# Performance work log

Measured on AMD Instinct MI355X. Metric: run time of the kernel, lower is better.

The kernel has to match this reference:

```python
import jax, jax.numpy as jnp
import numpy as np

P = 16          # patch size
D = 256         # emb dim
NH = 4          # attention heads
DH = D // NH    # head dim
GS = 4          # LE-fusion group size
EPS = 1e-5
ALPHA = 1.0
DELTA = 1.0
BETA = 1.0


def setup_inputs() -> dict:
    key = jax.random.key(0)
    ks = jax.random.split(key, 12)
    B, C, H, W = 8, 1, 256, 256
    s = 0.02
    return {
        "x": jax.random.normal(ks[0], (B, C, H, W), jnp.float32),
        # patch embed as matmul over flattened patches (equivalent to Conv2d k=s=P)
        "Wp": jax.random.normal(ks[1], (C * P * P, D), jnp.float32) * s,
        "bp": jnp.zeros((D,), jnp.float32),
        "ln_g": jnp.ones((D,), jnp.float32),
        "ln_b": jnp.zeros((D,), jnp.float32),
        "Wq": jax.random.normal(ks[2], (D, D), jnp.float32) * s,
        "bq": jnp.zeros((D,), jnp.float32),
        "Wk": jax.random.normal(ks[3], (D, D), jnp.float32) * s,
        "bk": jnp.zeros((D,), jnp.float32),
        "Wv": jax.random.normal(ks[4], (D, D), jnp.float32) * s,
        "bv": jnp.zeros((D,), jnp.float32),
        "Wo": jax.random.normal(ks[5], (D, D), jnp.float32) * s,
        "bo": jnp.zeros((D,), jnp.float32),
    }


def _forward(x, Wp, bp, ln_g, ln_b, Wq, bq, Wk, bk, Wv, bv, Wo, bo):
    B, C, H, W = x.shape
    nh, nw = H // P, W // P
    N = nh * nw
    # --- patch embed: (B,C,H,W) -> (B,N,C*P*P) @ Wp ---
    patches = x.reshape(B, C, nh, P, nw, P).transpose(0, 2, 4, 1, 3, 5)
    patches = patches.reshape(B, N, C * P * P)
    z = patches @ Wp + bp  # (B, N, D)
    # --- NF-Norm: LayerNorm then NeuroFocal scaling ---
    mu = z.mean(-1, keepdims=True)
    var = ((z - mu) ** 2).mean(-1, keepdims=True)
    zn = (z - mu) * jax.lax.rsqrt(var + EPS) * ln_g + ln_b
    mu2 = zn.mean(-1, keepdims=True)
    var2 = ((zn - mu2) ** 2).mean(-1, keepdims=True)
    nf = jnp.abs(zn - mu2).sum(-1, keepdims=True) / (jnp.sqrt(var2 + EPS) + EPS)
    z = zn * (1.0 + nf)
    # --- AG-NFA attention ---
    def split(t):  # (B,N,D) -> (B,NH,N,DH)
        return t.reshape(B, N, NH, DH).transpose(0, 2, 1, 3)
    Q = split(z @ Wq + bq)
    K = split(z @ Wk + bk)
    V = split(z @ Wv + bv)
    qk = jnp.einsum("bhnd,bhmd->bhnm", Q, K)
    logits = qk / jnp.sqrt(jnp.float32(DH))
    mu_q = Q.mean(-1, keepdims=True)
    var_q = ((Q - mu_q) ** 2).mean(-1, keepdims=True)
    sigma_q = jnp.sqrt(var_q + EPS)
    nf_q = jnp.abs(Q - mu_q).sum(-1, keepdims=True) / (sigma_q + EPS)  # (B,NH,N,1)
    # ||Q_n - K_m||^2 = |Q|^2 + |K|^2 - 2 Q.K  (avoids O(N^2*d) diff tensor)
    q2 = (Q * Q).sum(-1)  # (B,NH,N)
    k2 = (K * K).sum(-1)  # (B,NH,N)
    omega = q2[..., :, None] + k2[..., None, :] - 2.0 * qk
    omega = omega / (jnp.exp(-DELTA * nf_q) + 1.0)
    A = jax.nn.softmax(logits - ALPHA * omega, axis=-1)
    out = jnp.einsum("bhnm,bhmd->bhnd", A, V)
    out = out.transpose(0, 2, 1, 3).reshape(B, N, D)
    Y = out @ Wo + bo
    # --- LE-Fusion ---
    G = N // GS
    Yg = Y.reshape(B, G, GS, D)
    E = jnp.linalg.norm(Yg, axis=-1)  # (B,G,GS)
    lam = jax.nn.softmax(BETA * E, axis=-1)[..., None]
    return (lam * Yg).sum(axis=2)  # (B, G, D)


def reference(x, Wp, bp, ln_g, ln_b, Wq, bq, Wk, bk, Wv, bv, Wo, bo):
    return _forward(x, Wp, bp, ln_g, ln_b, Wq, bq, Wk, bk, Wv, bv, Wo, bo)
```

## Files before the change

### kernel.cpp

```cpp
#include <hip/hip_runtime.h>

#define EPSF 1e-5f
#define KSTR 68
#define PSTR 260

#define FMA4(ACC, ZS, WV) \
    ACC.x = fmaf(ZS, WV.x, ACC.x); ACC.y = fmaf(ZS, WV.y, ACC.y); \
    ACC.z = fmaf(ZS, WV.z, ACC.z); ACC.w = fmaf(ZS, WV.w, ACC.w);

__device__ __forceinline__ void gemm_pass8(
    const float* __restrict__ W, const float* __restrict__ zr,
    float* __restrict__ ps, int kq, int tg4, int ln)
{
    const float* wr = W + kq * 8192 + 4 * ln;
    const float* zb = zr + tg4 * 256 + kq * 32;
    float4 a0 = make_float4(0.f,0.f,0.f,0.f), a1 = a0, a2 = a0, a3 = a0;
    #pragma unroll
    for (int kk = 0; kk < 32; kk += 8) {
        float4 w0 = *(const float4*)(wr + (kk + 0) * 256);
        float4 w1 = *(const float4*)(wr + (kk + 1) * 256);
        float4 w2 = *(const float4*)(wr + (kk + 2) * 256);
        float4 w3 = *(const float4*)(wr + (kk + 3) * 256);
        float4 w4 = *(const float4*)(wr + (kk + 4) * 256);
        float4 w5 = *(const float4*)(wr + (kk + 5) * 256);
        float4 w6 = *(const float4*)(wr + (kk + 6) * 256);
        float4 w7 = *(const float4*)(wr + (kk + 7) * 256);
        float4 zA0 = *(const float4*)(zb + 0 * 256 + kk);
        float4 zA1 = *(const float4*)(zb + 0 * 256 + kk + 4);
        float4 zB0 = *(const float4*)(zb + 1 * 256 + kk);
        float4 zB1 = *(const float4*)(zb + 1 * 256 + kk + 4);
        float4 zC0 = *(const float4*)(zb + 2 * 256 + kk);
        float4 zC1 = *(const float4*)(zb + 2 * 256 + kk + 4);
        float4 zD0 = *(const float4*)(zb + 3 * 256 + kk);
        float4 zD1 = *(const float4*)(zb + 3 * 256 + kk + 4);
        FMA4(a0, zA0.x, w0) FMA4(a0, zA0.y, w1) FMA4(a0, zA0.z, w2) FMA4(a0, zA0.w, w3)
        FMA4(a0, zA1.x, w4) FMA4(a0, zA1.y, w5) FMA4(a0, zA1.z, w6) FMA4(a0, zA1.w, w7)
        FMA4(a1, zB0.x, w0) FMA4(a1, zB0.y, w1) FMA4(a1, zB0.z, w2) FMA4(a1, zB0.w, w3)
        FMA4(a1, zB1.x, w4) FMA4(a1, zB1.y, w5) FMA4(a1, zB1.z, w6) FMA4(a1, zB1.w, w7)
        FMA4(a2, zC0.x, w0) FMA4(a2, zC0.y, w1) FMA4(a2, zC0.z, w2) FMA4(a2, zC0.w, w3)
        FMA4(a2, zC1.x, w4) FMA4(a2, zC1.y, w5) FMA4(a2, zC1.z, w6) FMA4(a2, zC1.w, w7)
        FMA4(a3, zD0.x, w0) FMA4(a3, zD0.y, w1) FMA4(a3, zD0.z, w2) FMA4(a3, zD0.w, w3)
        FMA4(a3, zD1.x, w4) FMA4(a3, zD1.y, w5) FMA4(a3, zD1.z, w6) FMA4(a3, zD1.w, w7)
    }
    float* pp = ps + kq * 2048 + tg4 * 256 + 4 * ln;
    *(float4*)(pp + 0 * 256) = a0;
    *(float4*)(pp + 1 * 256) = a1;
    *(float4*)(pp + 2 * 256) = a2;
    *(float4*)(pp + 3 * 256) = a3;
}

__device__ __forceinline__ float4 combine8(const float* __restrict__ ps, int e)
{
    float4 a = *(const float4*)(ps + e);
    #pragma unroll
    for (int kq = 1; kq < 8; ++kq) {
        float4 u = *(const float4*)(ps + kq * 2048 + e);
        a.x += u.x; a.y += u.y; a.z += u.z; a.w += u.w;
    }
    return a;
}

__global__ __launch_bounds__(1024, 4) void ka_patch_nf_qkv(
    const float* __restrict__ x,
    const float* __restrict__ Wp, const float* __restrict__ bp,
    const float* __restrict__ ln_g, const float* __restrict__ ln_b,
    const float* __restrict__ Wq, const float* __restrict__ bq,
    const float* __restrict__ Wk, const float* __restrict__ bk,
    const float* __restrict__ Wv, const float* __restrict__ bv,
    float* __restrict__ Qg, float* __restrict__ Kg, float* __restrict__ Vg)
{
    extern __shared__ float sm[];
    float* zr = sm;
    float* ps = sm + 2048;

    const int tid = threadIdx.x;
    const int kq = tid >> 7, tg = (tid >> 6) & 1, ln = tid & 63;
    const int wave = tid >> 6, lane = tid & 63;
    const int tok0 = blockIdx.x * 8;
    const int tg4 = 4 * tg;

    {
        int e = tid * 2;
        int t = e >> 8, dd = e & 255;
        int tk = tok0 + t, b = tk >> 8, n = tk & 255;
        int ph = n >> 4, pw = n & 15, p = dd >> 4, q = dd & 15;
        float2 v = *(const float2*)(x + b * 65536 + (ph * 16 + p) * 256 + pw * 16 + q);
        *(float2*)(zr + e) = v;
    }
    __syncthreads();

    gemm_pass8(Wp, zr, ps, kq, tg4, ln);
    __syncthreads();
    if (tid < 512) {
        int e = tid * 4;
        float4 a = combine8(ps, e);
        float4 bb = *(const float4*)(bp + (e & 255));
        a.x += bb.x; a.y += bb.y; a.z += bb.z; a.w += bb.w;
        *(float4*)(zr + e) = a;
    }
    __syncthreads();

    if (wave < 8) {
        float g[4], bb2[4], v[4];
        #pragma unroll
        for (int c = 0; c < 4; ++c) { g[c] = ln_g[lane + 64 * c]; bb2[c] = ln_b[lane + 64 * c]; }
        float s = 0.f, ss = 0.f;
        #pragma unroll
        for (int c = 0; c < 4; ++c) { v[c] = zr[wave * 256 + lane + 64 * c]; s += v[c]; ss += v[c] * v[c]; }
        #pragma unroll
        for (int o = 32; o; o >>= 1) { s += __shfl_xor(s, o); ss += __shfl_xor(ss, o); }
        float mu  = s * (1.f / 256.f);
        float var = ss * (1.f / 256.f) - mu * mu;
        float rs  = rsqrtf(var + EPSF);
        float zn[4]; float s2 = 0.f, ss2 = 0.f;
        #pragma unroll
        for (int c = 0; c < 4; ++c) {
            zn[c] = (v[c] - mu) * rs * g[c] + bb2[c];
            s2 += zn[c]; ss2 += zn[c] * zn[c];
        }
        #pragma unroll
        for (int o = 32; o; o >>= 1) { s2 += __shfl_xor(s2, o); ss2 += __shfl_xor(ss2, o); }
        float mu2  = s2 * (1.f / 256.f);
        float var2 = ss2 * (1.f / 256.f) - mu2 * mu2;
        float as = 0.f;
        #pragma unroll
        for (int c = 0; c < 4; ++c) as += fabsf(zn[c] - mu2);
        #pragma unroll
        for (int o = 32; o; o >>= 1) as += __shfl_xor(as, o);
        float nf = as / (sqrtf(var2 + EPSF) + EPSF);
        float sc = 1.f + nf;
        #pragma unroll
        for (int c = 0; c < 4; ++c) zr[wave * 256 + lane + 64 * c] = zn[c] * sc;
    }
    __syncthreads();

    {
        int e = tid * 4, t = e >> 8, d0 = e & 255;
        int tk = tok0 + t, b = tk >> 8, n = tk & 255;
        int h = d0 >> 6, dh = d0 & 63;
        const long goff = ((long)(b * 4 + h) * 256 + n) * 64 + dh;

        gemm_pass8(Wq, zr, ps, kq, tg4, ln);
        __syncthreads();
        if (tid < 512) {
            float4 a = combine8(ps, e);
            float4 bb = *(const float4*)(bq + d0);
            a.x += bb.x; a.y += bb.y; a.z += bb.z; a.w += bb.w;
            *(float4*)(Qg + goff) = a;
        }
        __syncthreads();

        gemm_pass8(Wk, zr, ps, kq, tg4, ln);
        __syncthreads();
        if (tid < 512) {
            float4 a = combine8(ps, e);
            float4 bb = *(const float4*)(bk + d0);
            a.x += bb.x; a.y += bb.y; a.z += bb.z; a.w += bb.w;
            *(float4*)(Kg + goff) = a;
        }
        __syncthreads();

        gemm_pass8(Wv, zr, ps, kq, tg4, ln);
        __syncthreads();
        if (tid < 512) {
            float4 a = combine8(ps, e);
            float4 bb = *(const float4*)(bv + d0);
            a.x += bb.x; a.y += bb.y; a.z += bb.z; a.w += bb.w;
            *(float4*)(Vg + goff) = a;
        }
    }
}

__global__ __launch_bounds__(512, 2) void kb_attn(
    const float* __restrict__ Qg, const float* __restrict__ Kg,
    const float* __restrict__ Vg, float* __restrict__ Og)
{
    extern __shared__ float lds[];
    float* Kl = lds;
    float* k2 = lds + 256 * KSTR;
    float* Pl = lds;

    const int tid = threadIdx.x;
    const int xcd = blockIdx.x & 7, slot = blockIdx.x >> 3;
    const int bh = xcd * 4 + (slot >> 3);
    const int qt = slot & 7;

    const float* Qb = Qg + (bh * 256 + qt * 32) * 64;
    const float* Kb = Kg + bh * 16384;
    const float* Vb = Vg + bh * 16384;

    const int q = tid >> 4;
    const int r = tid & 15;

    {
        const float4* Ks = (const float4*)Kb;
        #pragma unroll
        for (int i = 0; i < 8; ++i) {
            int flat = tid + 512 * i;
            int row = flat >> 4, c4 = flat & 15;
            *(float4*)(Kl + row * KSTR + c4 * 4) = Ks[flat];
        }
    }
    __syncthreads();

    {
        int row = tid >> 1, half = tid & 1;
        const float* kp = Kl + row * KSTR + half * 32;
        float ssq = 0.f;
        #pragma unroll
        for (int c = 0; c < 8; ++c) {
            float4 kv = *(const float4*)(kp + 4 * c);
            ssq += kv.x*kv.x + kv.y*kv.y + kv.z*kv.z + kv.w*kv.w;
        }
        ssq += __shfl_xor(ssq, 1);
        if (half == 0) k2[row] = ssq;
    }

    float4 Qr[16];
    {
        const float4* Qp = (const float4*)(Qb + q * 64);
        #pragma unroll
        for (int c = 0; c < 16; ++c) Qr[c] = Qp[c];
    }
    float fq, gq, iq;
    {
        float s = 0.f, ss = 0.f;
        #pragma unroll
        for (int c = 0; c < 16; ++c) {
            float4 v = Qr[c];
            s  += v.x + v.y + v.z + v.w;
            ss += v.x*v.x + v.y*v.y + v.z*v.z + v.w*v.w;
        }
        float mu = s * (1.f / 64.f);
        float as = 0.f;
        #pragma unroll
        for (int c = 0; c < 16; ++c) {
            float4 v = Qr[c];
            as += fabsf(v.x - mu) + fabsf(v.y - mu)
                + fabsf(v.z - mu) + fabsf(v.w - mu);
        }
        float var = ss * (1.f / 64.f) - mu * mu;
        float sg  = sqrtf(var + EPSF);
        float nf  = as / (sg + EPSF);
        float inv = 1.f / (__expf(-nf) + 1.f);
        fq = 0.125f + 2.f * inv;
        gq = ss * inv;
        iq = inv;
    }
    __syncthreads();

    float s_[16];
    #pragma unroll
    for (int j = 0; j < 16; ++j) {
        int m = r + 16 * j;
        const float* kp = Kl + m * KSTR;
        float acc = 0.f;
        #pragma unroll
        for (int c = 0; c < 16; ++c) {
            float4 kv = *(const float4*)(kp + 4 * c);
            acc += Qr[c].x*kv.x + Qr[c].y*kv.y + Qr[c].z*kv.z + Qr[c].w*kv.w;
        }
        s_[j] = acc * fq - gq - k2[m] * iq;
    }

    float M = s_[0];
    #pragma unroll
    for (int j = 1; j < 16; ++j) M = fmaxf(M, s_[j]);
    #pragma unroll
    for (int o = 1; o < 16; o <<= 1) M = fmaxf(M, __shfl_xor(M, o));
    float L = 0.f;
    #pragma unroll
    for (int j = 0; j < 16; ++j) { s_[j] = __expf(s_[j] - M); L += s_[j]; }
    #pragma unroll
    for (int o = 1; o < 16; o <<= 1) L += __shfl_xor(L, o);
    float invL = 1.f / L;

    __syncthreads();
    #pragma unroll
    for (int j = 0; j < 16; ++j) Pl[q * PSTR + r + 16 * j] = s_[j] * invL;
    __syncthreads();

    float4 a0 = make_float4(0.f, 0.f, 0.f, 0.f);
    const float* pq = Pl + q * PSTR;
    #pragma unroll 8
    for (int m = 0; m < 256; ++m) {
        float pw = pq[m];
        float4 v = *(const float4*)(Vb + m * 64 + 4 * r);
        a0.x = fmaf(pw, v.x, a0.x); a0.y = fmaf(pw, v.y, a0.y);
        a0.z = fmaf(pw, v.z, a0.z); a0.w = fmaf(pw, v.w, a0.w);
    }
    {
        int b = bh >> 2, h = bh & 3;
        int n = qt * 32 + q;
        float* op = Og + (b * 256 + n) * 256 + h * 64 + 4 * r;
        *(float4*)op = a0;
    }
}

__global__ __launch_bounds__(1024, 4) void kc_wo_le(
    const float* __restrict__ Og, const float* __restrict__ Wo,
    const float* __restrict__ bo, float* __restrict__ out)
{
    extern __shared__ float sm[];
    float* yr  = sm;
    float* ps  = sm + 2048;
    float* red = sm + 18432;

    const int tid = threadIdx.x;
    const int kq = tid >> 7, tg = (tid >> 6) & 1, ln = tid & 63;
    const int wave = tid >> 6, lane = tid & 63;
    const int tok0 = blockIdx.x * 8;
    const int tg4 = 4 * tg;

    *(float2*)(yr + tid * 2) = *(const float2*)(Og + tok0 * 256 + tid * 2);
    __syncthreads();

    gemm_pass8(Wo, yr, ps, kq, tg4, ln);
    __syncthreads();
    if (tid < 512) {
        int e = tid * 4;
        float4 a = combine8(ps, e);
        float4 bb = *(const float4*)(bo + (e & 255));
        a.x += bb.x; a.y += bb.y; a.z += bb.z; a.w += bb.w;
        *(float4*)(yr + e) = a;
    }
    __syncthreads();
    if (wave < 8) {
        float ssq = 0.f;
        #pragma unroll
        for (int c = 0; c < 4; ++c) {
            float v = yr[wave * 256 + lane + 64 * c];
            ssq += v * v;
        }
        #pragma unroll
        for (int o = 32; o; o >>= 1) ssq += __shfl_xor(ssq, o);
        if (lane == 0) red[wave] = sqrtf(ssq);
    }
    __syncthreads();
    if (tid < 512) {
        int g = tid >> 8, d = tid & 255;
        float e0 = red[4 * g], e1 = red[4 * g + 1], e2 = red[4 * g + 2], e3 = red[4 * g + 3];
        float m = fmaxf(fmaxf(e0, e1), fmaxf(e2, e3));
        float x0 = __expf(e0 - m), x1 = __expf(e1 - m), x2 = __expf(e2 - m), x3 = __expf(e3 - m);
        float inv = 1.f / (x0 + x1 + x2 + x3);
        float val = (x0 * yr[(4 * g) * 256 + d] + x1 * yr[(4 * g + 1) * 256 + d]
                   + x2 * yr[(4 * g + 2) * 256 + d] + x3 * yr[(4 * g + 3) * 256 + d]) * inv;
        out[(blockIdx.x * 2 + g) * 256 + d] = val;
    }
}

extern "C" void kernel_launch(void* const* d_in, const int* in_sizes, int n_in,
                              void* d_out, int out_size, void* d_ws, size_t ws_size,
                              hipStream_t stream) {
    const float* x    = (const float*)d_in[0];
    const float* Wp   = (const float*)d_in[1];
    const float* bp   = (const float*)d_in[2];
    const float* ln_g = (const float*)d_in[3];
    const float* ln_b = (const float*)d_in[4];
    const float* Wq   = (const float*)d_in[5];
    const float* bq   = (const float*)d_in[6];
    const float* Wk   = (const float*)d_in[7];
    const float* bk   = (const float*)d_in[8];
    const float* Wv   = (const float*)d_in[9];
    const float* bv   = (const float*)d_in[10];
    const float* Wo   = (const float*)d_in[11];
    const float* bo   = (const float*)d_in[12];
    float* out = (float*)d_out;

    float* ws = (float*)d_ws;
    const size_t TKD = 2048 * 64 * 4;
    float* Qg = ws;
    float* Kg = ws + TKD;
    float* Vg = ws + 2 * TKD;
    float* Og = ws + 3 * TKD;

    const int ka_lds = (2048 + 16384) * 4;
    const int kb_lds = (256 * KSTR + 256) * 4;
    const int kc_lds = (2048 + 16384 + 8) * 4;
    (void)hipFuncSetAttribute((const void*)ka_patch_nf_qkv,
                              hipFuncAttributeMaxDynamicSharedMemorySize, ka_lds);
    (void)hipFuncSetAttribute((const void*)kb_attn,
                              hipFuncAttributeMaxDynamicSharedMemorySize, kb_lds);
    (void)hipFuncSetAttribute((const void*)kc_wo_le,
                              hipFuncAttributeMaxDynamicSharedMemorySize, kc_lds);

    ka_patch_nf_qkv<<<256, 1024, ka_lds, stream>>>(x, Wp, bp, ln_g, ln_b,
                                                   Wq, bq, Wk, bk, Wv, bv, Qg, Kg, Vg);
    kb_attn<<<256, 512, kb_lds, stream>>>(Qg, Kg, Vg, Og);
    kc_wo_le<<<256, 1024, kc_lds, stream>>>(Og, Wo, bo, out);
}
```

Measured before the change: 61.95 us.

## Halve block size in GEMM kernels with 8-token register tile per thread

The projection GEMM helper now has each thread accumulate all 8 tokens against its 4 output columns for one K-slice, instead of splitting the tokens across two thread groups. The patch/QKV and Wo/LE kernels launch with 512 threads instead of 1024, and the idle-thread guards in the reduction and normalisation stages are removed. Each weight vector loaded from global memory is now reused across 8 tokens, halving weight traffic per block and using all threads in the epilogues. In exchange each thread holds more accumulator registers and there are fewer threads per block to hide latency.

```diff
diff --git a/kernel.cpp b/kernel.cpp
--- a/kernel.cpp
+++ b/kernel.cpp
@@ -8,59 +8,60 @@
     ACC.x = fmaf(ZS, WV.x, ACC.x); ACC.y = fmaf(ZS, WV.y, ACC.y); \
     ACC.z = fmaf(ZS, WV.z, ACC.z); ACC.w = fmaf(ZS, WV.w, ACC.w);
 
-__device__ __forceinline__ void gemm_pass8(
+__device__ __forceinline__ void pass8x8(
     const float* __restrict__ W, const float* __restrict__ zr,
-    float* __restrict__ ps, int kq, int tg4, int ln)
+    float* __restrict__ ps, int kq, int ln)
 {
     const float* wr = W + kq * 8192 + 4 * ln;
-    const float* zb = zr + tg4 * 256 + kq * 32;
+    const float* zb = zr + kq * 32;
     float4 a0 = make_float4(0.f,0.f,0.f,0.f), a1 = a0, a2 = a0, a3 = a0;
-    #pragma unroll
-    for (int kk = 0; kk < 32; kk += 8) {
+    float4 a4 = a0, a5 = a0, a6 = a0, a7 = a0;
+    #pragma unroll
+    for (int kk = 0; kk < 32; kk += 4) {
         float4 w0 = *(const float4*)(wr + (kk + 0) * 256);
         float4 w1 = *(const float4*)(wr + (kk + 1) * 256);
         float4 w2 = *(const float4*)(wr + (kk + 2) * 256);
         float4 w3 = *(const float4*)(wr + (kk + 3) * 256);
-        float4 w4 = *(const float4*)(wr + (kk + 4) * 256);
-        float4 w5 = *(const float4*)(wr + (kk + 5) * 256);
-        float4 w6 = *(const float4*)(wr + (kk + 6) * 256);
-        float4 w7 = *(const float4*)(wr + (kk + 7) * 256);
-        float4 zA0 = *(const float4*)(zb + 0 * 256 + kk);
-        float4 zA1 = *(const float4*)(zb + 0 * 256 + kk + 4);
-        float4 zB0 = *(const float4*)(zb + 1 * 256 + kk);
-        float4 zB1 = *(const float4*)(zb + 1 * 256 + kk + 4);
-        float4 zC0 = *(const float4*)(zb + 2 * 256 + kk);
-        float4 zC1 = *(const float4*)(zb + 2 * 256 + kk + 4);
-        float4 zD0 = *(const float4*)(zb + 3 * 256 + kk);
-        float4 zD1 = *(const float4*)(zb + 3 * 256 + kk + 4);
-        FMA4(a0, zA0.x, w0) FMA4(a0, zA0.y, w1) FMA4(a0, zA0.z, w2) FMA4(a0, zA0.w, w3)
-        FMA4(a0, zA1.x, w4) FMA4(a0, zA1.y, w5) FMA4(a0, zA1.z, w6) FMA4(a0, zA1.w, w7)
-        FMA4(a1, zB0.x, w0) FMA4(a1, zB0.y, w1) FMA4(a1, zB0.z, w2) FMA4(a1, zB0.w, w3)
-        FMA4(a1, zB1.x, w4) FMA4(a1, zB1.y, w5) FMA4(a1, zB1.z, w6) FMA4(a1, zB1.w, w7)
-        FMA4(a2, zC0.x, w0) FMA4(a2, zC0.y, w1) FMA4(a2, zC0.z, w2) FMA4(a2, zC0.w, w3)
-        FMA4(a2, zC1.x, w4) FMA4(a2, zC1.y, w5) FMA4(a2, zC1.z, w6) FMA4(a2, zC1.w, w7)
-        FMA4(a3, zD0.x, w0) FMA4(a3, zD0.y, w1) FMA4(a3, zD0.z, w2) FMA4(a3, zD0.w, w3)
-        FMA4(a3, zD1.x, w4) FMA4(a3, zD1.y, w5) FMA4(a3, zD1.z, w6) FMA4(a3, zD1.w, w7)
-    }
-    float* pp = ps + kq * 2048 + tg4 * 256 + 4 * ln;
+        float4 z0 = *(const float4*)(zb + 0 * 256 + kk);
+        float4 z1 = *(const float4*)(zb + 1 * 256 + kk);
+        float4 z2 = *(const float4*)(zb + 2 * 256 + kk);
+        float4 z3 = *(const float4*)(zb + 3 * 256 + kk);
+        float4 z4 = *(const float4*)(zb + 4 * 256 + kk);
+        float4 z5 = *(const float4*)(zb + 5 * 256 + kk);
+        float4 z6 = *(const float4*)(zb + 6 * 256 + kk);
+        float4 z7 = *(const float4*)(zb + 7 * 256 + kk);
+        FMA4(a0, z0.x, w0) FMA4(a0, z0.y, w1) FMA4(a0, z0.z, w2) FMA4(a0, z0.w, w3)
+        FMA4(a1, z1.x, w0) FMA4(a1, z1.y, w1) FMA4(a1, z1.z, w2) FMA4(a1, z1.w, w3)
+        FMA4(a2, z2.x, w0) FMA4(a2, z2.y, w1) FMA4(a2, z2.z, w2) FMA4(a2, z2.w, w3)
+        FMA4(a3, z3.x, w0) FMA4(a3, z3.y, w1) FMA4(a3, z3.z, w2) FMA4(a3, z3.w, w3)
+        FMA4(a4, z4.x, w0) FMA4(a4, z4.y, w1) FMA4(a4, z4.z, w2) FMA4(a4, z4.w, w3)
+        FMA4(a5, z5.x, w0) FMA4(a5, z5.y, w1) FMA4(a5, z5.z, w2) FMA4(a5, z5.w, w3)
+        FMA4(a6, z6.x, w0) FMA4(a6, z6.y, w1) FMA4(a6, z6.z, w2) FMA4(a6, z6.w, w3)
+        FMA4(a7, z7.x, w0) FMA4(a7, z7.y, w1) FMA4(a7, z7.z, w2) FMA4(a7, z7.w, w3)
+    }
+    float* pp = ps + kq * 2048 + 4 * ln;
     *(float4*)(pp + 0 * 256) = a0;
     *(float4*)(pp + 1 * 256) = a1;
     *(float4*)(pp + 2 * 256) = a2;
     *(float4*)(pp + 3 * 256) = a3;
+    *(float4*)(pp + 4 * 256) = a4;
+    *(float4*)(pp + 5 * 256) = a5;
+    *(float4*)(pp + 6 * 256) = a6;
+    *(float4*)(pp + 7 * 256) = a7;
 }
 
 __device__ __forceinline__ float4 combine8(const float* __restrict__ ps, int e)
 {
     float4 a = *(const float4*)(ps + e);
     #pragma unroll
-    for (int kq = 1; kq < 8; ++kq) {
-        float4 u = *(const float4*)(ps + kq * 2048 + e);
+    for (int k = 1; k < 8; ++k) {
+        float4 u = *(const float4*)(ps + k * 2048 + e);
         a.x += u.x; a.y += u.y; a.z += u.z; a.w += u.w;
     }
     return a;
 }
 
-__global__ __launch_bounds__(1024, 4) void ka_patch_nf_qkv(
+__global__ __launch_bounds__(512, 2) void ka_patch_nf_qkv(
     const float* __restrict__ x,
     const float* __restrict__ Wp, const float* __restrict__ bp,
     const float* __restrict__ ln_g, const float* __restrict__ ln_b,
@@ -74,24 +75,23 @@
     float* ps = sm + 2048;
 
     const int tid = threadIdx.x;
-    const int kq = tid >> 7, tg = (tid >> 6) & 1, ln = tid & 63;
+    const int kq = tid >> 6, ln = tid & 63;
     const int wave = tid >> 6, lane = tid & 63;
     const int tok0 = blockIdx.x * 8;
-    const int tg4 = 4 * tg;
-
-    {
-        int e = tid * 2;
+
+    #pragma unroll
+    for (int i = 0; i < 4; ++i) {
+        int e = tid + 512 * i;
         int t = e >> 8, dd = e & 255;
         int tk = tok0 + t, b = tk >> 8, n = tk & 255;
         int ph = n >> 4, pw = n & 15, p = dd >> 4, q = dd & 15;
-        float2 v = *(const float2*)(x + b * 65536 + (ph * 16 + p) * 256 + pw * 16 + q);
-        *(float2*)(zr + e) = v;
-    }
-    __syncthreads();
-
-    gemm_pass8(Wp, zr, ps, kq, tg4, ln);
-    __syncthreads();
-    if (tid < 512) {
+        zr[t * 256 + dd] = x[b * 65536 + (ph * 16 + p) * 256 + pw * 16 + q];
+    }
+    __syncthreads();
+
+    pass8x8(Wp, zr, ps, kq, ln);
+    __syncthreads();
+    {
         int e = tid * 4;
         float4 a = combine8(ps, e);
         float4 bb = *(const float4*)(bp + (e & 255));
@@ -100,7 +100,7 @@
     }
     __syncthreads();
 
-    if (wave < 8) {
+    {
         float g[4], bb2[4], v[4];
         #pragma unroll
         for (int c = 0; c < 4; ++c) { g[c] = ln_g[lane + 64 * c]; bb2[c] = ln_b[lane + 64 * c]; }
@@ -140,9 +140,9 @@
         int h = d0 >> 6, dh = d0 & 63;
         const long goff = ((long)(b * 4 + h) * 256 + n) * 64 + dh;
 
-        gemm_pass8(Wq, zr, ps, kq, tg4, ln);
-        __syncthreads();
-        if (tid < 512) {
+        pass8x8(Wq, zr, ps, kq, ln);
+        __syncthreads();
+        {
             float4 a = combine8(ps, e);
             float4 bb = *(const float4*)(bq + d0);
             a.x += bb.x; a.y += bb.y; a.z += bb.z; a.w += bb.w;
@@ -150,9 +150,9 @@
         }
         __syncthreads();
 
-        gemm_pass8(Wk, zr, ps, kq, tg4, ln);
-        __syncthreads();
-        if (tid < 512) {
+        pass8x8(Wk, zr, ps, kq, ln);
+        __syncthreads();
+        {
             float4 a = combine8(ps, e);
             float4 bb = *(const float4*)(bk + d0);
             a.x += bb.x; a.y += bb.y; a.z += bb.z; a.w += bb.w;
@@ -160,9 +160,9 @@
         }
         __syncthreads();
 
-        gemm_pass8(Wv, zr, ps, kq, tg4, ln);
-        __syncthreads();
-        if (tid < 512) {
+        pass8x8(Wv, zr, ps, kq, ln);
+        __syncthreads();
+        {
             float4 a = combine8(ps, e);
             float4 bb = *(const float4*)(bv + d0);
             a.x += bb.x; a.y += bb.y; a.z += bb.z; a.w += bb.w;
@@ -297,7 +297,7 @@
     }
 }
 
-__global__ __launch_bounds__(1024, 4) void kc_wo_le(
+__global__ __launch_bounds__(512, 2) void kc_wo_le(
     const float* __restrict__ Og, const float* __restrict__ Wo,
     const float* __restrict__ bo, float* __restrict__ out)
 {
@@ -307,17 +307,16 @@
     float* red = sm + 18432;
 
     const int tid = threadIdx.x;
-    const int kq = tid >> 7, tg = (tid >> 6) & 1, ln = tid & 63;
+    const int kq = tid >> 6, ln = tid & 63;
     const int wave = tid >> 6, lane = tid & 63;
     const int tok0 = blockIdx.x * 8;
-    const int tg4 = 4 * tg;
-
-    *(float2*)(yr + tid * 2) = *(const float2*)(Og + tok0 * 256 + tid * 2);
-    __syncthreads();
-
-    gemm_pass8(Wo, yr, ps, kq, tg4, ln);
-    __syncthreads();
-    if (tid < 512) {
+
+    *(float4*)(yr + tid * 4) = *(const float4*)(Og + tok0 * 256 + tid * 4);
+    __syncthreads();
+
+    pass8x8(Wo, yr, ps, kq, ln);
+    __syncthreads();
+    {
         int e = tid * 4;
         float4 a = combine8(ps, e);
         float4 bb = *(const float4*)(bo + (e & 255));
@@ -325,7 +324,7 @@
         *(float4*)(yr + e) = a;
     }
     __syncthreads();
-    if (wave < 8) {
+    {
         float ssq = 0.f;
         #pragma unroll
         for (int c = 0; c < 4; ++c) {
@@ -337,7 +336,7 @@
         if (lane == 0) red[wave] = sqrtf(ssq);
     }
     __syncthreads();
-    if (tid < 512) {
+    {
         int g = tid >> 8, d = tid & 255;
         float e0 = red[4 * g], e1 = red[4 * g + 1], e2 = red[4 * g + 2], e3 = red[4 * g + 3];
         float m = fmaxf(fmaxf(e0, e1), fmaxf(e2, e3));
@@ -368,11 +367,10 @@
     float* out = (float*)d_out;
 
     float* ws = (float*)d_ws;
-    const size_t TKD = 2048 * 64 * 4;
     float* Qg = ws;
-    float* Kg = ws + TKD;
-    float* Vg = ws + 2 * TKD;
-    float* Og = ws + 3 * TKD;
+    float* Kg = ws + 524288;
+    float* Vg = ws + 524288 * 2;
+    float* Og = ws + 524288 * 3;
 
     const int ka_lds = (2048 + 16384) * 4;
     const int kb_lds = (256 * KSTR + 256) * 4;
@@ -384,8 +382,8 @@
     (void)hipFuncSetAttribute((const void*)kc_wo_le,
                               hipFuncAttributeMaxDynamicSharedMemorySize, kc_lds);
 
-    ka_patch_nf_qkv<<<256, 1024, ka_lds, stream>>>(x, Wp, bp, ln_g, ln_b,
-                                                   Wq, bq, Wk, bk, Wv, bv, Qg, Kg, Vg);
+    ka_patch_nf_qkv<<<256, 512, ka_lds, stream>>>(x, Wp, bp, ln_g, ln_b,
+                                                  Wq, bq, Wk, bk, Wv, bv, Qg, Kg, Vg);
     kb_attn<<<256, 512, kb_lds, stream>>>(Qg, Kg, Vg, Og);
-    kc_wo_le<<<256, 1024, kc_lds, stream>>>(Og, Wo, bo, out);
-}
+    kc_wo_le<<<256, 512, kc_lds, stream>>>(Og, Wo, bo, out);
+}
```

Measured after the change: 57.48 us. 7.2% less time.
